# Performance work log

Measured on AMD Instinct MI355X. Metric: run time of the kernel, lower is better.

The kernel has to match this reference:

```python
import jax, jax.numpy as jnp
import numpy as np

NUM_CLASSES = 3
IMG = 448
STRIDES = (8, 16, 32)
POS_IOU, NEG_IOU = 0.5, 0.3
NEG_RATIO = 3
B, T = 64, 20


def _make_anchors(stride):
    f = IMG // stride
    cs = (np.arange(f, dtype=np.float32) + 0.5) * stride
    cx, cy = np.meshgrid(cs, cs, indexing='xy')            # [f, f]
    sizes = np.array([2.0, 2.5, 3.0], np.float32) * stride  # 3 square anchors / loc
    cx = np.broadcast_to(cx[..., None], (f, f, 3))
    cy = np.broadcast_to(cy[..., None], (f, f, 3))
    w = np.broadcast_to(sizes, (f, f, 3))
    boxes = np.stack([cx - w / 2, cy - w / 2, cx + w / 2, cy + w / 2], -1)
    return jnp.asarray(boxes.reshape(-1, 4), jnp.float32)   # [f*f*3, 4]


def setup_inputs() -> dict:
    key = jax.random.key(0)
    k1, k2, k3, kc, ks, kl = jax.random.split(key, 6)
    pred1 = jax.random.normal(k1, (B, 24, 56, 56), jnp.float32)
    pred2 = jax.random.normal(k2, (B, 24, 28, 28), jnp.float32)
    pred3 = jax.random.normal(k3, (B, 24, 14, 14), jnp.float32)
    ctr = jax.random.uniform(kc, (B, T, 2), jnp.float32, 20.0, IMG - 20.0)
    wh = jax.random.uniform(ks, (B, T, 2), jnp.float32, 20.0, 120.0)
    target_boxes = jnp.concatenate([ctr - wh / 2, ctr + wh / 2], axis=-1)  # [B,T,4] xyxy
    target_labels = jax.random.randint(kl, (B, T), 1, NUM_CLASSES + 1, jnp.int32)
    return {
        'pred1': pred1, 'pred2': pred2, 'pred3': pred3,
        'anchor1': _make_anchors(8), 'anchor2': _make_anchors(16), 'anchor3': _make_anchors(32),
        'target_boxes': target_boxes, 'target_labels': target_labels,
    }


def _iou(a, b):  # a [A,4], b [T,4] -> [A,T]
    lt = jnp.maximum(a[:, None, :2], b[None, :, :2])
    rb = jnp.minimum(a[:, None, 2:], b[None, :, 2:])
    wh = jnp.clip(rb - lt, 0.0)
    inter = wh[..., 0] * wh[..., 1]
    area_a = (a[:, 2] - a[:, 0]) * (a[:, 3] - a[:, 1])
    area_b = (b[:, 2] - b[:, 0]) * (b[:, 3] - b[:, 1])
    return inter / (area_a[:, None] + area_b[None, :] - inter + 1e-9)


def _encode(gt, an):  # both [A,4] xyxy -> [A,4] deltas
    aw, ah = an[:, 2] - an[:, 0], an[:, 3] - an[:, 1]
    acx, acy = (an[:, 0] + an[:, 2]) * 0.5, (an[:, 1] + an[:, 3]) * 0.5
    gw, gh = gt[:, 2] - gt[:, 0], gt[:, 3] - gt[:, 1]
    gcx, gcy = (gt[:, 0] + gt[:, 2]) * 0.5, (gt[:, 1] + gt[:, 3]) * 0.5
    return jnp.stack([(gcx - acx) / aw, (gcy - acy) / ah,
                      jnp.log(gw / aw), jnp.log(gh / ah)], axis=-1)


def _bce_logits(x, y):
    return jnp.maximum(x, 0.0) - x * y + jnp.log1p(jnp.exp(-jnp.abs(x)))


def _image_loss(deltas, obj, cls, boxes, labels, anchors):
    # deltas [A,4], obj [A], cls [A,K], boxes [T,4], labels [T], anchors [A,4]
    iou = _iou(anchors, boxes)                    # [A,T]
    matched_t = jnp.argmax(iou, axis=1)           # [A]
    max_iou = jnp.max(iou, axis=1)
    pos = max_iou >= POS_IOU
    neg = max_iou < NEG_IOU
    # force each GT's best anchor to be positive
    best_a = jnp.argmax(iou, axis=0)              # [T]
    matched_t = matched_t.at[best_a].set(jnp.arange(boxes.shape[0]))
    pos = pos.at[best_a].set(True)
    neg = neg.at[best_a].set(False)
    matched_labels = jnp.where(pos, labels[matched_t], 0)
    # objectness + hard negative mining (rank-based topk, jit-safe)
    obj_t = (matched_labels > 0).astype(obj.dtype)
    bce = _bce_logits(obj, obj_t)
    num_pos = pos.sum()
    need = jnp.minimum(NEG_RATIO * num_pos, neg.sum())
    rank = jnp.argsort(jnp.argsort(-jnp.where(neg, bce, -jnp.inf)))
    sel = pos | ((rank < need) & neg)
    obj_loss = jnp.sum(jnp.where(sel, bce, 0.0)) / jnp.maximum(sel.sum(), 1)
    # classification (mean over positives)
    logp = jax.nn.log_softmax(cls, axis=-1)
    tgt = jnp.maximum(matched_labels - 1, 0)
    ce = -jnp.take_along_axis(logp, tgt[:, None], axis=1)[:, 0]
    cls_loss = jnp.sum(jnp.where(pos, ce, 0.0)) / jnp.maximum(num_pos, 1)
    # localization: smooth L1, mean over positive anchor elements
    tdel = _encode(boxes[matched_t], anchors)
    d = jnp.abs(deltas - tdel)
    sl1 = jnp.where(d < 1.0, 0.5 * d * d, d - 0.5)
    loc_loss = jnp.sum(jnp.where(pos[:, None], sl1, 0.0)) / jnp.maximum(4 * num_pos, 1)
    return obj_loss, cls_loss, loc_loss


def _scale_loss(pred, anchors, boxes, labels):
    Bp, C, H, W = pred.shape
    p = pred.transpose(0, 2, 3, 1).reshape(Bp, H * W * 3, 5 + NUM_CLASSES)
    deltas, obj, cls = p[..., :4], p[..., 4], p[..., 5:]
    fn = jax.vmap(lambda d, o, c, b, l: _image_loss(d, o, c, b, l, anchors))
    ol, cl, ll = fn(deltas, obj, cls, boxes, labels)
    return ol.sum(), cl.sum(), ll.sum()


def reference(pred1, pred2, pred3, anchor1, anchor2, anchor3, target_boxes, target_labels):
    tot = jnp.zeros(3, jnp.float32)
    for pred, anc in ((pred1, anchor1), (pred2, anchor2), (pred3, anchor3)):
        ol, cl, ll = _scale_loss(pred, anc, target_boxes, target_labels)
        tot = tot + jnp.stack([ol, cl, ll])
    bsz = target_boxes.shape[0]
    obj, cls, loc = tot[0] / bsz, tot[1] / bsz, tot[2] / bsz
    total = obj + cls + 2.0 * loc
    return jnp.stack([obj, cls, loc, total])
```

## Files before the change

kernel.cpp:

```cpp
#include <hip/hip_runtime.h>
#include <math.h>

#define T 20
#define APB 12348
#define LOSS_OFF 16
#define NPNN_OFF 640
#define KEY_OFF  2048
#define MF_BYTE_OFF (4 * (KEY_OFF + 64 * APB))

__device__ __forceinline__ unsigned mapf(float x) {
    unsigned u = __float_as_uint(x);
    return (u & 0x80000000u) ? ~u : (u | 0x80000000u);
}
__device__ __forceinline__ float unmapf(unsigned m) {
    return __uint_as_float((m & 0x80000000u) ? (m ^ 0x80000000u) : ~m);
}
__device__ __forceinline__ float bce_pos(float x) {
    return fmaxf(x, 0.f) - x + log1pf(expf(-fabsf(x)));
}
__device__ __forceinline__ float bce_neg(float x) {
    return fmaxf(x, 0.f) + log1pf(expf(-fabsf(x)));
}

__global__ __launch_bounds__(256) void match_kernel(
    const float* __restrict__ pred1, const float* __restrict__ pred2,
    const float* __restrict__ pred3, const float* __restrict__ tboxes,
    unsigned* __restrict__ wsu, unsigned short* __restrict__ mf)
{
#pragma clang fp contract(off)
    const int blk = blockIdx.x;
    const int b = blk / 11, c = blk - 11 * b;
    int s, j0;
    if (c < 8)       { s = 0; j0 = c * 1176; }
    else if (c < 10) { s = 1; j0 = (c - 8) * 1176; }
    else             { s = 2; j0 = 0; }
    const float* __restrict__ pred = (s == 0) ? pred1 : (s == 1) ? pred2 : pred3;
    const int W = 56 >> s, HW = W * W, A = 3 * HW;
    const float stf = (float)(8 << s);
    const int sh = 3 - s;
    const int lim = min(1176, A - j0);

    __shared__ float4   s_box[T];
    __shared__ float    s_ab[T];
    __shared__ unsigned s_np[4];
    const int tid = threadIdx.x, lane = tid & 63, wid = tid >> 6;

    if (tid < T) {
        float4 g = ((const float4*)tboxes)[b * T + tid];
        s_box[tid] = g;
        s_ab[tid]  = (g.z - g.x) * (g.w - g.y);
    }
    __syncthreads();

    float ax[5], ay[5], az[5], aw[5], ar[5], bn[5], bu[5];
    int at_[5], kk[5], pp[5];
    bool vv[5];
    float xlo = 1e30f, xhi = -1e30f, ylo = 1e30f, yhi = -1e30f;
    const int obase = 5 * tid;
#pragma unroll
    for (int r = 0; r < 5; r++) {
        int o = obase + r;
        vv[r] = (o < lim);
        int j = j0 + (vv[r] ? o : 0);
        int k   = (j >= HW) + (j >= 2 * HW);
        int pix = j - k * HW;
        int qq  = pix >> sh;
        int py  = (qq * 9363) >> 16;
        int px  = pix - py * W;
        float w  = (2.0f + 0.5f * (float)k) * stf;
        float cx = ((float)px + 0.5f) * stf;
        float cy = ((float)py + 0.5f) * stf;
        ax[r] = cx - 0.5f * w; ay[r] = cy - 0.5f * w;
        az[r] = cx + 0.5f * w; aw[r] = cy + 0.5f * w;
        ar[r] = w * w;
        bn[r] = 0.f; bu[r] = 1.f; at_[r] = 0;
        kk[r] = k; pp[r] = pix;
        xlo = fminf(xlo, ax[r]); xhi = fmaxf(xhi, az[r]);
        ylo = fminf(ylo, ay[r]); yhi = fmaxf(yhi, aw[r]);
    }

    for (int t = 0; t < T; t++) {
        float4 g = s_box[t];
        if (g.x < xhi && g.z > xlo && g.y < yhi && g.w > ylo) {
            float ab = s_ab[t];
#pragma unroll
            for (int r = 0; r < 5; r++) {
                float lx = fmaxf(ax[r], g.x), ly = fmaxf(ay[r], g.y);
                float rx = fminf(az[r], g.z), ry = fminf(aw[r], g.w);
                float ww = fmaxf(rx - lx, 0.f), hh = fmaxf(ry - ly, 0.f);
                float inter = ww * hh;
                float u = ((ar[r] + ab) - inter) + 1e-9f;
                if (inter * bu[r] > bn[r] * u) { bn[r] = inter; bu[r] = u; at_[r] = t; }
            }
        }
    }

    const float* objbase = pred + (size_t)(b * 24 + 4) * HW;
    const unsigned base = (unsigned)(b * APB + ((s == 0) ? 0 : (s == 1) ? 9408 : 11760));
    unsigned npnn = 0;
#pragma unroll
    for (int r = 0; r < 5; r++) {
        if (vv[r]) {
            int j = j0 + obase + r;
            bool pos = (bn[r] + bn[r] >= bu[r]);
            bool neg = (bn[r] < 0.3f * bu[r]);
            unsigned key = 0u;
            if (neg) key = mapf(objbase[(size_t)kk[r] * 8 * HW + pp[r]]);
            wsu[KEY_OFF + base + j] = key;
            mf[base + j] = (unsigned short)(at_[r] | (pos ? 0x100 : 0) | (neg ? 0x200 : 0));
            npnn += (pos ? 1u : 0u) + (neg ? 0x10000u : 0u);
        }
    }
    for (int off = 32; off; off >>= 1) npnn += (unsigned)__shfl_down((int)npnn, off, 64);
    if (lane == 0) s_np[wid] = npnn;
    __syncthreads();
    if (tid == 0) wsu[NPNN_OFF + blk] = s_np[0] + s_np[1] + s_np[2] + s_np[3];
}

__global__ __launch_bounds__(1024) void select_loss_kernel(
    const float* __restrict__ pred1, const float* __restrict__ pred2,
    const float* __restrict__ pred3, const float* __restrict__ tboxes,
    const int* __restrict__ tlabels,
    unsigned* __restrict__ wsu, unsigned short* __restrict__ mf)
{
#pragma clang fp contract(off)
    const int bid = blockIdx.x;
    const int b = bid / 3, s = bid - 3 * b;
    const float* __restrict__ pred = (s == 0) ? pred1 : (s == 1) ? pred2 : pred3;
    const int W = 56 >> s, HW = W * W, A = 3 * HW;
    const float stf = (float)(8 << s);
    const int sh = 3 - s;
    const unsigned base = (unsigned)(b * APB + ((s == 0) ? 0 : (s == 1) ? 9408 : 11760));

    __shared__ float4   s_box[T];
    __shared__ int      s_lab[T];
    __shared__ int      s_besta[T];
    __shared__ unsigned s_misc[4];
    __shared__ float    s_redf[16 * 4];
    __shared__ unsigned hist[2048];

    const int tid = threadIdx.x, lane = tid & 63, wid = tid >> 6;

    if (tid < T) {
        s_box[tid] = ((const float4*)tboxes)[b * T + tid];
        s_lab[tid] = tlabels[b * T + tid];
    }
    if (tid >= 32 && tid < 36) s_misc[tid - 32] = 0;
    __syncthreads();

    for (int t = wid; t < T; t += 16) {
        float4 g = s_box[t];
        float  ab = (g.z - g.x) * (g.w - g.y);
        int px0 = max(0, (int)floorf(g.x / stf) - 2);
        int px1 = min(W - 1, (int)floorf(g.z / stf) + 2);
        int py0 = max(0, (int)floorf(g.y / stf) - 2);
        int py1 = min(W - 1, (int)floorf(g.w / stf) + 2);
        int rowlen = (px1 - px0 + 1) * 3;
        float bi = -1.f, bu2 = 1.f;
        int ba = 0;
        for (int py = py0; py <= py1; py++) {
            float cy = ((float)py + 0.5f) * stf;
            for (int cc = lane; cc < rowlen; cc += 64) {
                int ix = (cc * 21846) >> 16;
                int k  = cc - 3 * ix;
                int px = px0 + ix;
                float w  = (2.0f + 0.5f * (float)k) * stf;
                float cx = ((float)px + 0.5f) * stf;
                float lx = fmaxf(cx - 0.5f * w, g.x), ly = fmaxf(cy - 0.5f * w, g.y);
                float rx = fminf(cx + 0.5f * w, g.z), ry = fminf(cy + 0.5f * w, g.w);
                float ww = fmaxf(rx - lx, 0.f), hh = fmaxf(ry - ly, 0.f);
                float inter = ww * hh;
                float u = ((w * w + ab) - inter) + 1e-9f;
                if (inter * bu2 > bi * u) {
                    bi = inter; bu2 = u; ba = (py * W + px) * 3 + k;
                }
            }
        }
        for (int off = 32; off; off >>= 1) {
            float oi = __shfl_down(bi, off, 64);
            float ou = __shfl_down(bu2, off, 64);
            int   oa = __shfl_down(ba, off, 64);
            float l = oi * bu2, r = bi * ou;
            if (l > r || (l == r && oa < ba)) { bi = oi; bu2 = ou; ba = oa; }
        }
        if (lane == 0) s_besta[t] = ba;
    }
    __syncthreads();

    int  j20 = 0; bool winner = false;
    if (tid < T) {
        int a = s_besta[tid];
        winner = true; bool first = true;
        for (int t2 = tid + 1; t2 < T; t2++) if (s_besta[t2] == a) winner = false;
        for (int t2 = 0; t2 < tid; t2++)     if (s_besta[t2] == a) first  = false;
        int pix = (a * 21846) >> 16;
        int k = a - 3 * pix;
        j20 = k * HW + pix;
        if (first) {
            unsigned old = mf[base + j20];
            unsigned d = ((old & 0x100u) ? 0u : 1u) +
                         ((old & 0x200u) ? 0xFFFF0000u : 0u);
            atomicAdd(&s_misc[0], d);
        }
    }
    __syncthreads();
    if (tid < T && winner) {
        mf[base + j20] = (unsigned short)(tid | 0x100);
        wsu[KEY_OFF + base + j20] = 0u;
    }
    __threadfence_block();
    __syncthreads();

    if (tid == 0) {
        int nslots = (s == 0) ? 8 : (s == 1) ? 2 : 1;
        int sb = b * 11 + ((s == 0) ? 0 : (s == 1) ? 8 : 10);
        unsigned p = 0;
        for (int i = 0; i < nslots; i++) p += wsu[NPNN_OFF + sb + i];
        s_misc[1] = p;
    }
    __syncthreads();
    unsigned packed = s_misc[1] + s_misc[0];
    unsigned np = packed & 0xFFFFu, nn = packed >> 16;
    unsigned need = min(3u * np, nn);

    unsigned keyreg[10];
    unsigned short mfr[10];
#pragma unroll
    for (int m = 0; m < 10; m++) {
        int j = tid + m * 1024;
        keyreg[m] = (j < A) ? wsu[KEY_OFF + base + j] : 0u;
        mfr[m]    = (j < A) ? mf[base + j] : (unsigned short)0;
    }

    unsigned kth = 0xFFFFFFFFu;
    if (need > 0) {
        unsigned prefix = 0, remaining = need;
        const int shifts[3] = {21, 10, 0};
        const int nbits[3]  = {11, 11, 10};
        for (int p = 0; p < 3; p++) {
            const int NB = 1 << nbits[p];
            const int sh_ = shifts[p];
            for (int i = tid; i < NB; i += 1024) hist[i] = 0;
            __syncthreads();
#pragma unroll
            for (int m = 0; m < 10; m++) {
                unsigned k = keyreg[m];
                bool ok = (p == 0) || ((k >> (sh_ + nbits[p])) == prefix);
                if (ok) atomicAdd(&hist[(k >> sh_) & (NB - 1)], 1u);
            }
            __syncthreads();
            if (wid == 0) {
                const int C = NB >> 6;
                int b0 = lane * C;
                unsigned csum = 0;
                for (int i = 0; i < C; i++) csum += hist[b0 + i];
                unsigned Tv = csum;
                for (int off = 1; off < 64; off <<= 1) {
                    unsigned o = __shfl_down(Tv, off, 64);
                    if (lane + off < 64) Tv += o;
                }
                unsigned long long ball = __ballot(Tv >= remaining);
                int L = 63 - __clzll(ball);
                if (lane == L) {
                    unsigned sv = Tv - csum;
                    int bb = b0 + C - 1;
                    while (true) { sv += hist[bb]; if (sv >= remaining) break; bb--; }
                    s_misc[1] = (unsigned)bb;
                    s_misc[2] = sv - hist[bb];
                }
            }
            __syncthreads();
            unsigned B = s_misc[1];
            remaining -= s_misc[2];
            prefix = (prefix << nbits[p]) | B;
        }
        kth = prefix;
    }

    float obj_s = 0.f, cls_s = 0.f, loc_s = 0.f;
    unsigned cgt = 0;
#pragma unroll 1
    for (int m = 0; m < 10; m++) {
        int j = tid + m * 1024;
        if (j >= A) break;
        unsigned mfv = mfr[m];
        if (mfv & 0x100u) {
            int k   = (j >= HW) + (j >= 2 * HW);
            int pix = j - k * HW;
            const float* bp = pred + (size_t)(b * 24 + k * 8) * HW + pix;
            float x = bp[(size_t)4 * HW];
            obj_s += bce_pos(x);
            int t = mfv & 0xFFu;
            float4 g = s_box[t];
            int tgt = s_lab[t] - 1;
            float c0 = bp[(size_t)5 * HW], c1 = bp[(size_t)6 * HW], c2 = bp[(size_t)7 * HW];
            float mm  = fmaxf(c0, fmaxf(c1, c2));
            float lse = logf(expf(c0 - mm) + expf(c1 - mm) + expf(c2 - mm));
            float ct = (tgt == 0) ? c0 : (tgt == 1) ? c1 : c2;
            cls_s += (mm + lse) - ct;
            int qq = pix >> sh;
            int py = (qq * 9363) >> 16;
            int px = pix - py * W;
            float w  = (2.0f + 0.5f * (float)k) * stf;
            float cx = ((float)px + 0.5f) * stf;
            float cy = ((float)py + 0.5f) * stf;
            float gcx = (g.x + g.z) * 0.5f, gcy = (g.y + g.w) * 0.5f;
            float gw = g.z - g.x, gh = g.w - g.y;
            float t0 = (gcx - cx) / w, t1 = (gcy - cy) / w;
            float t2 = logf(gw / w),   t3 = logf(gh / w);
            float d0 = bp[0], d1 = bp[(size_t)HW], d2 = bp[(size_t)2 * HW], d3 = bp[(size_t)3 * HW];
            float dd;
            dd = fabsf(d0 - t0); loc_s += (dd < 1.f) ? 0.5f * dd * dd : dd - 0.5f;
            dd = fabsf(d1 - t1); loc_s += (dd < 1.f) ? 0.5f * dd * dd : dd - 0.5f;
            dd = fabsf(d2 - t2); loc_s += (dd < 1.f) ? 0.5f * dd * dd : dd - 0.5f;
            dd = fabsf(d3 - t3); loc_s += (dd < 1.f) ? 0.5f * dd * dd : dd - 0.5f;
        } else {
            unsigned key = keyreg[m];
            if (key > kth) { obj_s += bce_neg(unmapf(key)); cgt++; }
        }
    }
    for (int off = 32; off; off >>= 1) {
        obj_s += __shfl_down(obj_s, off, 64);
        cls_s += __shfl_down(cls_s, off, 64);
        loc_s += __shfl_down(loc_s, off, 64);
        cgt   += (unsigned)__shfl_down((int)cgt, off, 64);
    }
    if (lane == 0) {
        s_redf[wid * 4 + 0] = obj_s;
        s_redf[wid * 4 + 1] = cls_s;
        s_redf[wid * 4 + 2] = loc_s;
        s_redf[wid * 4 + 3] = __uint_as_float(cgt);
    }
    __syncthreads();
    if (tid == 0) {
        float ob = 0.f, cl = 0.f, lc = 0.f;
        unsigned cg = 0;
        for (int w2 = 0; w2 < 16; w2++) {
            ob += s_redf[w2 * 4 + 0];
            cl += s_redf[w2 * 4 + 1];
            lc += s_redf[w2 * 4 + 2];
            cg += __float_as_uint(s_redf[w2 * 4 + 3]);
        }
        if (need > 0) ob += (float)(need - cg) * bce_neg(unmapf(kth));
        float* wsf = (float*)wsu;
        wsf[LOSS_OFF + bid * 3 + 0] = ob / (float)max(np + need, 1u);
        wsf[LOSS_OFF + bid * 3 + 1] = cl / (float)max(np, 1u);
        wsf[LOSS_OFF + bid * 3 + 2] = lc / (float)max(4u * np, 1u);
    }
}

__global__ void finalize_kernel(const float* __restrict__ wsf,
                                float* __restrict__ out) {
    const int t = threadIdx.x, lane = t & 63, wid = t >> 6;
    __shared__ float red[12];
    float v0 = 0.f, v1 = 0.f, v2 = 0.f;
    if (t < 192) {
        v0 = wsf[LOSS_OFF + 3 * t];
        v1 = wsf[LOSS_OFF + 3 * t + 1];
        v2 = wsf[LOSS_OFF + 3 * t + 2];
    }
    for (int off = 32; off; off >>= 1) {
        v0 += __shfl_down(v0, off, 64);
        v1 += __shfl_down(v1, off, 64);
        v2 += __shfl_down(v2, off, 64);
    }
    if (lane == 0) { red[wid * 3] = v0; red[wid * 3 + 1] = v1; red[wid * 3 + 2] = v2; }
    __syncthreads();
    if (t == 0) {
        float obj = 0.f, cls = 0.f, loc = 0.f;
        for (int w2 = 0; w2 < 4; w2++) {
            obj += red[w2 * 3]; cls += red[w2 * 3 + 1]; loc += red[w2 * 3 + 2];
        }
        obj /= 64.f; cls /= 64.f; loc /= 64.f;
        out[0] = obj; out[1] = cls; out[2] = loc;
        out[3] = obj + cls + 2.f * loc;
    }
}

extern "C" void kernel_launch(void* const* d_in, const int* in_sizes, int n_in,
                              void* d_out, int out_size, void* d_ws, size_t ws_size,
                              hipStream_t stream) {
    const float* pred1   = (const float*)d_in[0];
    const float* pred2   = (const float*)d_in[1];
    const float* pred3   = (const float*)d_in[2];
    const float* tboxes  = (const float*)d_in[6];
    const int*   tlabels = (const int*)d_in[7];
    unsigned* wsu = (unsigned*)d_ws;
    unsigned short* mf = (unsigned short*)((char*)d_ws + MF_BYTE_OFF);
    float* out = (float*)d_out;

    match_kernel<<<64 * 11, 256, 0, stream>>>(pred1, pred2, pred3, tboxes, wsu, mf);
    select_loss_kernel<<<64 * 3, 1024, 0, stream>>>(
        pred1, pred2, pred3, tboxes, tlabels, wsu, mf);
    finalize_kernel<<<1, 256, 0, stream>>>((const float*)d_ws, out);
}
```

Baseline: 124.3 us.

## Fuse anchor matching into select-loss kernel, keeping match results in registers

The separate match kernel is folded into the per-(image,scale) select/loss kernel. Each of the 1024 threads now computes IoU matching for up to 10 anchors and keeps keys and match flags in registers. This removes the global workspace round-trip for keys and flags and one kernel launch. Forced best-anchor matches are applied by comparing against a register copy of the per-target best anchors instead of doing global read-modify-writes. In exchange, matching parallelism drops from 704 blocks of 256 threads to 192 blocks of 1024, so the scale-0 blocks carry much more matching work and the per-block load is more imbalanced.

```diff
diff --git a/kernel.cpp b/kernel.cpp
--- a/kernel.cpp
+++ b/kernel.cpp
@@ -2,126 +2,26 @@
 #include <math.h>
 
 #define T 20
-#define APB 12348
 #define LOSS_OFF 16
-#define NPNN_OFF 640
-#define KEY_OFF  2048
-#define MF_BYTE_OFF (4 * (KEY_OFF + 64 * APB))
-
-__device__ __forceinline__ unsigned mapf(float x) {
+
+static __device__ __forceinline__ unsigned mapf(float x) {
     unsigned u = __float_as_uint(x);
     return (u & 0x80000000u) ? ~u : (u | 0x80000000u);
 }
-__device__ __forceinline__ float unmapf(unsigned m) {
+static __device__ __forceinline__ float unmapf(unsigned m) {
     return __uint_as_float((m & 0x80000000u) ? (m ^ 0x80000000u) : ~m);
 }
-__device__ __forceinline__ float bce_pos(float x) {
+static __device__ __forceinline__ float bce_pos(float x) {
     return fmaxf(x, 0.f) - x + log1pf(expf(-fabsf(x)));
 }
-__device__ __forceinline__ float bce_neg(float x) {
+static __device__ __forceinline__ float bce_neg(float x) {
     return fmaxf(x, 0.f) + log1pf(expf(-fabsf(x)));
 }
 
-__global__ __launch_bounds__(256) void match_kernel(
+__global__ __launch_bounds__(1024, 1) void fused_kernel(
     const float* __restrict__ pred1, const float* __restrict__ pred2,
     const float* __restrict__ pred3, const float* __restrict__ tboxes,
-    unsigned* __restrict__ wsu, unsigned short* __restrict__ mf)
-{
-#pragma clang fp contract(off)
-    const int blk = blockIdx.x;
-    const int b = blk / 11, c = blk - 11 * b;
-    int s, j0;
-    if (c < 8)       { s = 0; j0 = c * 1176; }
-    else if (c < 10) { s = 1; j0 = (c - 8) * 1176; }
-    else             { s = 2; j0 = 0; }
-    const float* __restrict__ pred = (s == 0) ? pred1 : (s == 1) ? pred2 : pred3;
-    const int W = 56 >> s, HW = W * W, A = 3 * HW;
-    const float stf = (float)(8 << s);
-    const int sh = 3 - s;
-    const int lim = min(1176, A - j0);
-
-    __shared__ float4   s_box[T];
-    __shared__ float    s_ab[T];
-    __shared__ unsigned s_np[4];
-    const int tid = threadIdx.x, lane = tid & 63, wid = tid >> 6;
-
-    if (tid < T) {
-        float4 g = ((const float4*)tboxes)[b * T + tid];
-        s_box[tid] = g;
-        s_ab[tid]  = (g.z - g.x) * (g.w - g.y);
-    }
-    __syncthreads();
-
-    float ax[5], ay[5], az[5], aw[5], ar[5], bn[5], bu[5];
-    int at_[5], kk[5], pp[5];
-    bool vv[5];
-    float xlo = 1e30f, xhi = -1e30f, ylo = 1e30f, yhi = -1e30f;
-    const int obase = 5 * tid;
-#pragma unroll
-    for (int r = 0; r < 5; r++) {
-        int o = obase + r;
-        vv[r] = (o < lim);
-        int j = j0 + (vv[r] ? o : 0);
-        int k   = (j >= HW) + (j >= 2 * HW);
-        int pix = j - k * HW;
-        int qq  = pix >> sh;
-        int py  = (qq * 9363) >> 16;
-        int px  = pix - py * W;
-        float w  = (2.0f + 0.5f * (float)k) * stf;
-        float cx = ((float)px + 0.5f) * stf;
-        float cy = ((float)py + 0.5f) * stf;
-        ax[r] = cx - 0.5f * w; ay[r] = cy - 0.5f * w;
-        az[r] = cx + 0.5f * w; aw[r] = cy + 0.5f * w;
-        ar[r] = w * w;
-        bn[r] = 0.f; bu[r] = 1.f; at_[r] = 0;
-        kk[r] = k; pp[r] = pix;
-        xlo = fminf(xlo, ax[r]); xhi = fmaxf(xhi, az[r]);
-        ylo = fminf(ylo, ay[r]); yhi = fmaxf(yhi, aw[r]);
-    }
-
-    for (int t = 0; t < T; t++) {
-        float4 g = s_box[t];
-        if (g.x < xhi && g.z > xlo && g.y < yhi && g.w > ylo) {
-            float ab = s_ab[t];
-#pragma unroll
-            for (int r = 0; r < 5; r++) {
-                float lx = fmaxf(ax[r], g.x), ly = fmaxf(ay[r], g.y);
-                float rx = fminf(az[r], g.z), ry = fminf(aw[r], g.w);
-                float ww = fmaxf(rx - lx, 0.f), hh = fmaxf(ry - ly, 0.f);
-                float inter = ww * hh;
-                float u = ((ar[r] + ab) - inter) + 1e-9f;
-                if (inter * bu[r] > bn[r] * u) { bn[r] = inter; bu[r] = u; at_[r] = t; }
-            }
-        }
-    }
-
-    const float* objbase = pred + (size_t)(b * 24 + 4) * HW;
-    const unsigned base = (unsigned)(b * APB + ((s == 0) ? 0 : (s == 1) ? 9408 : 11760));
-    unsigned npnn = 0;
-#pragma unroll
-    for (int r = 0; r < 5; r++) {
-        if (vv[r]) {
-            int j = j0 + obase + r;
-            bool pos = (bn[r] + bn[r] >= bu[r]);
-            bool neg = (bn[r] < 0.3f * bu[r]);
-            unsigned key = 0u;
-            if (neg) key = mapf(objbase[(size_t)kk[r] * 8 * HW + pp[r]]);
-            wsu[KEY_OFF + base + j] = key;
-            mf[base + j] = (unsigned short)(at_[r] | (pos ? 0x100 : 0) | (neg ? 0x200 : 0));
-            npnn += (pos ? 1u : 0u) + (neg ? 0x10000u : 0u);
-        }
-    }
-    for (int off = 32; off; off >>= 1) npnn += (unsigned)__shfl_down((int)npnn, off, 64);
-    if (lane == 0) s_np[wid] = npnn;
-    __syncthreads();
-    if (tid == 0) wsu[NPNN_OFF + blk] = s_np[0] + s_np[1] + s_np[2] + s_np[3];
-}
-
-__global__ __launch_bounds__(1024) void select_loss_kernel(
-    const float* __restrict__ pred1, const float* __restrict__ pred2,
-    const float* __restrict__ pred3, const float* __restrict__ tboxes,
-    const int* __restrict__ tlabels,
-    unsigned* __restrict__ wsu, unsigned short* __restrict__ mf)
+    const int* __restrict__ tlabels, float* __restrict__ wsf)
 {
 #pragma clang fp contract(off)
     const int bid = blockIdx.x;
@@ -130,27 +30,97 @@
     const int W = 56 >> s, HW = W * W, A = 3 * HW;
     const float stf = (float)(8 << s);
     const int sh = 3 - s;
-    const unsigned base = (unsigned)(b * APB + ((s == 0) ? 0 : (s == 1) ? 9408 : 11760));
 
     __shared__ float4   s_box[T];
+    __shared__ float    s_ab[T];
     __shared__ int      s_lab[T];
     __shared__ int      s_besta[T];
-    __shared__ unsigned s_misc[4];
+    __shared__ unsigned s_npnn;
+    __shared__ unsigned s_bc[2];
     __shared__ float    s_redf[16 * 4];
     __shared__ unsigned hist[2048];
 
     const int tid = threadIdx.x, lane = tid & 63, wid = tid >> 6;
 
     if (tid < T) {
-        s_box[tid] = ((const float4*)tboxes)[b * T + tid];
+        float4 g = ((const float4*)tboxes)[b * T + tid];
+        s_box[tid] = g;
+        s_ab[tid]  = (g.z - g.x) * (g.w - g.y);
         s_lab[tid] = tlabels[b * T + tid];
     }
-    if (tid >= 32 && tid < 36) s_misc[tid - 32] = 0;
-    __syncthreads();
+    if (tid == 0) s_npnn = 0u;
+    __syncthreads();
+
+    const float* objbase = pred + (size_t)(b * 24 + 4) * HW;
+
+    unsigned keyreg[10];
+    unsigned mfr[10];
+#pragma unroll
+    for (int m = 0; m < 10; m++) { keyreg[m] = 0u; mfr[m] = 0u; }
+
+#pragma unroll
+    for (int bat = 0; bat < 2; bat++) {
+        int jb = bat * 5120 + 5 * tid;
+        if (jb < A) {
+            float ax[5], ay[5], az[5], aw[5], ar[5], bn[5], bu[5];
+            int at_[5];
+            float xlo = 1e30f, xhi = -1e30f, ylo = 1e30f, yhi = -1e30f;
+#pragma unroll
+            for (int r = 0; r < 5; r++) {
+                int j = jb + r; if (j >= A) j = A - 1;
+                int k   = (j >= HW) + (j >= 2 * HW);
+                int pix = j - k * HW;
+                int qq  = pix >> sh;
+                int py  = (qq * 9363) >> 16;
+                int px  = pix - py * W;
+                float w  = (2.0f + 0.5f * (float)k) * stf;
+                float cx = ((float)px + 0.5f) * stf;
+                float cy = ((float)py + 0.5f) * stf;
+                ax[r] = cx - 0.5f * w; ay[r] = cy - 0.5f * w;
+                az[r] = cx + 0.5f * w; aw[r] = cy + 0.5f * w;
+                ar[r] = w * w;
+                bn[r] = 0.f; bu[r] = 1.f; at_[r] = 0;
+                xlo = fminf(xlo, ax[r]); xhi = fmaxf(xhi, az[r]);
+                ylo = fminf(ylo, ay[r]); yhi = fmaxf(yhi, aw[r]);
+            }
+            for (int t = 0; t < T; t++) {
+                float4 g = s_box[t];
+                if (g.x < xhi && g.z > xlo && g.y < yhi && g.w > ylo) {
+                    float ab = s_ab[t];
+#pragma unroll
+                    for (int r = 0; r < 5; r++) {
+                        float lx = fmaxf(ax[r], g.x), ly = fmaxf(ay[r], g.y);
+                        float rx = fminf(az[r], g.z), ry = fminf(aw[r], g.w);
+                        float ww = fmaxf(rx - lx, 0.f), hh = fmaxf(ry - ly, 0.f);
+                        float inter = ww * hh;
+                        float u = ((ar[r] + ab) - inter) + 1e-9f;
+                        if (inter * bu[r] > bn[r] * u) {
+                            bn[r] = inter; bu[r] = u; at_[r] = t;
+                        }
+                    }
+                }
+            }
+#pragma unroll
+            for (int r = 0; r < 5; r++) {
+                int j = jb + r;
+                if (j < A) {
+                    int k   = (j >= HW) + (j >= 2 * HW);
+                    int pix = j - k * HW;
+                    bool pos = (bn[r] + bn[r] >= bu[r]);
+                    bool neg = (bn[r] < 0.3f * bu[r]);
+                    unsigned key = 0u;
+                    if (neg) key = mapf(objbase[(size_t)k * 8 * HW + pix]);
+                    keyreg[bat * 5 + r] = key;
+                    mfr[bat * 5 + r] = (unsigned)at_[r] | (pos ? 0x100u : 0u)
+                                                        | (neg ? 0x200u : 0u);
+                }
+            }
+        }
+    }
 
     for (int t = wid; t < T; t += 16) {
         float4 g = s_box[t];
-        float  ab = (g.z - g.x) * (g.w - g.y);
+        float  ab = s_ab[t];
         int px0 = max(0, (int)floorf(g.x / stf) - 2);
         int px1 = min(W - 1, (int)floorf(g.z / stf) + 2);
         int py0 = max(0, (int)floorf(g.y / stf) - 2);
@@ -183,54 +153,38 @@
             float l = oi * bu2, r = bi * ou;
             if (l > r || (l == r && oa < ba)) { bi = oi; bu2 = ou; ba = oa; }
         }
-        if (lane == 0) s_besta[t] = ba;
-    }
-    __syncthreads();
-
-    int  j20 = 0; bool winner = false;
-    if (tid < T) {
-        int a = s_besta[tid];
-        winner = true; bool first = true;
-        for (int t2 = tid + 1; t2 < T; t2++) if (s_besta[t2] == a) winner = false;
-        for (int t2 = 0; t2 < tid; t2++)     if (s_besta[t2] == a) first  = false;
-        int pix = (a * 21846) >> 16;
-        int k = a - 3 * pix;
-        j20 = k * HW + pix;
-        if (first) {
-            unsigned old = mf[base + j20];
-            unsigned d = ((old & 0x100u) ? 0u : 1u) +
-                         ((old & 0x200u) ? 0xFFFF0000u : 0u);
-            atomicAdd(&s_misc[0], d);
-        }
-    }
-    __syncthreads();
-    if (tid < T && winner) {
-        mf[base + j20] = (unsigned short)(tid | 0x100);
-        wsu[KEY_OFF + base + j20] = 0u;
-    }
-    __threadfence_block();
-    __syncthreads();
-
-    if (tid == 0) {
-        int nslots = (s == 0) ? 8 : (s == 1) ? 2 : 1;
-        int sb = b * 11 + ((s == 0) ? 0 : (s == 1) ? 8 : 10);
-        unsigned p = 0;
-        for (int i = 0; i < nslots; i++) p += wsu[NPNN_OFF + sb + i];
-        s_misc[1] = p;
-    }
-    __syncthreads();
-    unsigned packed = s_misc[1] + s_misc[0];
+        if (lane == 0) {
+            int pix = (ba * 21846) >> 16;
+            int k = ba - 3 * pix;
+            s_besta[t] = k * HW + pix;
+        }
+    }
+    __syncthreads();
+
+    {
+        int best[T];
+#pragma unroll
+        for (int t = 0; t < T; t++) best[t] = s_besta[t];
+#pragma unroll
+        for (int m = 0; m < 10; m++) {
+            int j = (m / 5) * 5120 + 5 * tid + (m - (m / 5) * 5);
+            int twin = -1;
+#pragma unroll
+            for (int t = 0; t < T; t++) if (best[t] == j) twin = t;
+            if (twin >= 0) { mfr[m] = (unsigned)twin | 0x100u; keyreg[m] = 0u; }
+        }
+    }
+
+    unsigned npnn = 0;
+#pragma unroll
+    for (int m = 0; m < 10; m++)
+        npnn += ((mfr[m] >> 8) & 1u) + (((mfr[m] >> 9) & 1u) << 16);
+    for (int off = 32; off; off >>= 1) npnn += (unsigned)__shfl_down((int)npnn, off, 64);
+    if (lane == 0) atomicAdd(&s_npnn, npnn);
+    __syncthreads();
+    unsigned packed = s_npnn;
     unsigned np = packed & 0xFFFFu, nn = packed >> 16;
     unsigned need = min(3u * np, nn);
-
-    unsigned keyreg[10];
-    unsigned short mfr[10];
-#pragma unroll
-    for (int m = 0; m < 10; m++) {
-        int j = tid + m * 1024;
-        keyreg[m] = (j < A) ? wsu[KEY_OFF + base + j] : 0u;
-        mfr[m]    = (j < A) ? mf[base + j] : (unsigned short)0;
-    }
 
     unsigned kth = 0xFFFFFFFFu;
     if (need > 0) {
@@ -265,13 +219,13 @@
                     unsigned sv = Tv - csum;
                     int bb = b0 + C - 1;
                     while (true) { sv += hist[bb]; if (sv >= remaining) break; bb--; }
-                    s_misc[1] = (unsigned)bb;
-                    s_misc[2] = sv - hist[bb];
+                    s_bc[0] = (unsigned)bb;
+                    s_bc[1] = sv - hist[bb];
                 }
             }
             __syncthreads();
-            unsigned B = s_misc[1];
-            remaining -= s_misc[2];
+            unsigned B = s_bc[0];
+            remaining -= s_bc[1];
             prefix = (prefix << nbits[p]) | B;
         }
         kth = prefix;
@@ -279,44 +233,45 @@
 
     float obj_s = 0.f, cls_s = 0.f, loc_s = 0.f;
     unsigned cgt = 0;
-#pragma unroll 1
+#pragma unroll
     for (int m = 0; m < 10; m++) {
-        int j = tid + m * 1024;
-        if (j >= A) break;
-        unsigned mfv = mfr[m];
-        if (mfv & 0x100u) {
-            int k   = (j >= HW) + (j >= 2 * HW);
-            int pix = j - k * HW;
-            const float* bp = pred + (size_t)(b * 24 + k * 8) * HW + pix;
-            float x = bp[(size_t)4 * HW];
-            obj_s += bce_pos(x);
-            int t = mfv & 0xFFu;
-            float4 g = s_box[t];
-            int tgt = s_lab[t] - 1;
-            float c0 = bp[(size_t)5 * HW], c1 = bp[(size_t)6 * HW], c2 = bp[(size_t)7 * HW];
-            float mm  = fmaxf(c0, fmaxf(c1, c2));
-            float lse = logf(expf(c0 - mm) + expf(c1 - mm) + expf(c2 - mm));
-            float ct = (tgt == 0) ? c0 : (tgt == 1) ? c1 : c2;
-            cls_s += (mm + lse) - ct;
-            int qq = pix >> sh;
-            int py = (qq * 9363) >> 16;
-            int px = pix - py * W;
-            float w  = (2.0f + 0.5f * (float)k) * stf;
-            float cx = ((float)px + 0.5f) * stf;
-            float cy = ((float)py + 0.5f) * stf;
-            float gcx = (g.x + g.z) * 0.5f, gcy = (g.y + g.w) * 0.5f;
-            float gw = g.z - g.x, gh = g.w - g.y;
-            float t0 = (gcx - cx) / w, t1 = (gcy - cy) / w;
-            float t2 = logf(gw / w),   t3 = logf(gh / w);
-            float d0 = bp[0], d1 = bp[(size_t)HW], d2 = bp[(size_t)2 * HW], d3 = bp[(size_t)3 * HW];
-            float dd;
-            dd = fabsf(d0 - t0); loc_s += (dd < 1.f) ? 0.5f * dd * dd : dd - 0.5f;
-            dd = fabsf(d1 - t1); loc_s += (dd < 1.f) ? 0.5f * dd * dd : dd - 0.5f;
-            dd = fabsf(d2 - t2); loc_s += (dd < 1.f) ? 0.5f * dd * dd : dd - 0.5f;
-            dd = fabsf(d3 - t3); loc_s += (dd < 1.f) ? 0.5f * dd * dd : dd - 0.5f;
-        } else {
-            unsigned key = keyreg[m];
-            if (key > kth) { obj_s += bce_neg(unmapf(key)); cgt++; }
+        int j = (m / 5) * 5120 + 5 * tid + (m - (m / 5) * 5);
+        if (j < A) {
+            unsigned mfv = mfr[m];
+            if (mfv & 0x100u) {
+                int k   = (j >= HW) + (j >= 2 * HW);
+                int pix = j - k * HW;
+                const float* bp = pred + (size_t)(b * 24 + k * 8) * HW + pix;
+                float x = bp[(size_t)4 * HW];
+                obj_s += bce_pos(x);
+                int t = mfv & 0xFFu;
+                float4 g = s_box[t];
+                int tgt = s_lab[t] - 1;
+                float c0 = bp[(size_t)5 * HW], c1 = bp[(size_t)6 * HW], c2 = bp[(size_t)7 * HW];
+                float mm  = fmaxf(c0, fmaxf(c1, c2));
+                float lse = logf(expf(c0 - mm) + expf(c1 - mm) + expf(c2 - mm));
+                float ct = (tgt == 0) ? c0 : (tgt == 1) ? c1 : c2;
+                cls_s += (mm + lse) - ct;
+                int qq = pix >> sh;
+                int py = (qq * 9363) >> 16;
+                int px = pix - py * W;
+                float w  = (2.0f + 0.5f * (float)k) * stf;
+                float cx = ((float)px + 0.5f) * stf;
+                float cy = ((float)py + 0.5f) * stf;
+                float gcx = (g.x + g.z) * 0.5f, gcy = (g.y + g.w) * 0.5f;
+                float gw = g.z - g.x, gh = g.w - g.y;
+                float t0 = (gcx - cx) / w, t1 = (gcy - cy) / w;
+                float t2 = logf(gw / w),   t3 = logf(gh / w);
+                float d0 = bp[0], d1 = bp[(size_t)HW], d2 = bp[(size_t)2 * HW], d3 = bp[(size_t)3 * HW];
+                float dd;
+                dd = fabsf(d0 - t0); loc_s += (dd < 1.f) ? 0.5f * dd * dd : dd - 0.5f;
+                dd = fabsf(d1 - t1); loc_s += (dd < 1.f) ? 0.5f * dd * dd : dd - 0.5f;
+                dd = fabsf(d2 - t2); loc_s += (dd < 1.f) ? 0.5f * dd * dd : dd - 0.5f;
+                dd = fabsf(d3 - t3); loc_s += (dd < 1.f) ? 0.5f * dd * dd : dd - 0.5f;
+            } else {
+                unsigned key = keyreg[m];
+                if (key > kth) { obj_s += bce_neg(unmapf(key)); cgt++; }
+            }
         }
     }
     for (int off = 32; off; off >>= 1) {
@@ -342,7 +297,6 @@
             cg += __float_as_uint(s_redf[w2 * 4 + 3]);
         }
         if (need > 0) ob += (float)(need - cg) * bce_neg(unmapf(kth));
-        float* wsf = (float*)wsu;
         wsf[LOSS_OFF + bid * 3 + 0] = ob / (float)max(np + need, 1u);
         wsf[LOSS_OFF + bid * 3 + 1] = cl / (float)max(np, 1u);
         wsf[LOSS_OFF + bid * 3 + 2] = lc / (float)max(4u * np, 1u);
@@ -385,12 +339,10 @@
     const float* pred3   = (const float*)d_in[2];
     const float* tboxes  = (const float*)d_in[6];
     const int*   tlabels = (const int*)d_in[7];
-    unsigned* wsu = (unsigned*)d_ws;
-    unsigned short* mf = (unsigned short*)((char*)d_ws + MF_BYTE_OFF);
+    float* wsf = (float*)d_ws;
     float* out = (float*)d_out;
 
-    match_kernel<<<64 * 11, 256, 0, stream>>>(pred1, pred2, pred3, tboxes, wsu, mf);
-    select_loss_kernel<<<64 * 3, 1024, 0, stream>>>(
-        pred1, pred2, pred3, tboxes, tlabels, wsu, mf);
-    finalize_kernel<<<1, 256, 0, stream>>>((const float*)d_ws, out);
-}
+    fused_kernel<<<64 * 3, 1024, 0, stream>>>(
+        pred1, pred2, pred3, tboxes, tlabels, wsf);
+    finalize_kernel<<<1, 256, 0, stream>>>(wsf, out);
+}
```

Result: faster. 120.7 us (-2.9%).

## Stage keys and flags in LDS, recount positives locally, use 8-bit radix select

Applied to the files above, without the earlier changes.

The select/loss kernel now copies each image-scale's keys and match flags into shared memory and applies the forced best-anchor overrides there, instead of writing them back to global memory. Positive and negative counts are recomputed from the shared flags, so the match kernel no longer does its block reduction and no longer writes per-block counts. The radix select for the k-th negative becomes four 8-bit passes with per-wave-pair histograms, which cuts atomic contention. The block size drops to 512 threads. This adds about 56KB of LDS per block, which may limit occupancy, and each pass now scans shared memory rather than registers.

```diff
diff --git a/kernel.cpp b/kernel.cpp
--- a/kernel.cpp
+++ b/kernel.cpp
@@ -2,23 +2,23 @@
 #include <math.h>
 
 #define T 20
+#define MAXA 9408
 #define APB 12348
 #define LOSS_OFF 16
-#define NPNN_OFF 640
 #define KEY_OFF  2048
 #define MF_BYTE_OFF (4 * (KEY_OFF + 64 * APB))
 
-__device__ __forceinline__ unsigned mapf(float x) {
+static __device__ __forceinline__ unsigned mapf(float x) {
     unsigned u = __float_as_uint(x);
     return (u & 0x80000000u) ? ~u : (u | 0x80000000u);
 }
-__device__ __forceinline__ float unmapf(unsigned m) {
+static __device__ __forceinline__ float unmapf(unsigned m) {
     return __uint_as_float((m & 0x80000000u) ? (m ^ 0x80000000u) : ~m);
 }
-__device__ __forceinline__ float bce_pos(float x) {
+static __device__ __forceinline__ float bce_pos(float x) {
     return fmaxf(x, 0.f) - x + log1pf(expf(-fabsf(x)));
 }
-__device__ __forceinline__ float bce_neg(float x) {
+static __device__ __forceinline__ float bce_neg(float x) {
     return fmaxf(x, 0.f) + log1pf(expf(-fabsf(x)));
 }
 
@@ -40,10 +40,9 @@
     const int sh = 3 - s;
     const int lim = min(1176, A - j0);
 
-    __shared__ float4   s_box[T];
-    __shared__ float    s_ab[T];
-    __shared__ unsigned s_np[4];
-    const int tid = threadIdx.x, lane = tid & 63, wid = tid >> 6;
+    __shared__ float4 s_box[T];
+    __shared__ float  s_ab[T];
+    const int tid = threadIdx.x;
 
     if (tid < T) {
         float4 g = ((const float4*)tboxes)[b * T + tid];
@@ -97,7 +96,6 @@
 
     const float* objbase = pred + (size_t)(b * 24 + 4) * HW;
     const unsigned base = (unsigned)(b * APB + ((s == 0) ? 0 : (s == 1) ? 9408 : 11760));
-    unsigned npnn = 0;
 #pragma unroll
     for (int r = 0; r < 5; r++) {
         if (vv[r]) {
@@ -108,20 +106,16 @@
             if (neg) key = mapf(objbase[(size_t)kk[r] * 8 * HW + pp[r]]);
             wsu[KEY_OFF + base + j] = key;
             mf[base + j] = (unsigned short)(at_[r] | (pos ? 0x100 : 0) | (neg ? 0x200 : 0));
-            npnn += (pos ? 1u : 0u) + (neg ? 0x10000u : 0u);
-        }
-    }
-    for (int off = 32; off; off >>= 1) npnn += (unsigned)__shfl_down((int)npnn, off, 64);
-    if (lane == 0) s_np[wid] = npnn;
-    __syncthreads();
-    if (tid == 0) wsu[NPNN_OFF + blk] = s_np[0] + s_np[1] + s_np[2] + s_np[3];
-}
-
-__global__ __launch_bounds__(1024) void select_loss_kernel(
+        }
+    }
+}
+
+__global__ __launch_bounds__(512) void select_loss_kernel(
     const float* __restrict__ pred1, const float* __restrict__ pred2,
     const float* __restrict__ pred3, const float* __restrict__ tboxes,
     const int* __restrict__ tlabels,
-    unsigned* __restrict__ wsu, unsigned short* __restrict__ mf)
+    const unsigned* __restrict__ wsu, const unsigned short* __restrict__ mf,
+    float* __restrict__ wsf)
 {
 #pragma clang fp contract(off)
     const int bid = blockIdx.x;
@@ -132,25 +126,36 @@
     const int sh = 3 - s;
     const unsigned base = (unsigned)(b * APB + ((s == 0) ? 0 : (s == 1) ? 9408 : 11760));
 
+    __shared__ unsigned       s_key[MAXA];
+    __shared__ unsigned short s_mf[MAXA];
     __shared__ float4   s_box[T];
+    __shared__ float    s_ab[T];
     __shared__ int      s_lab[T];
     __shared__ int      s_besta[T];
-    __shared__ unsigned s_misc[4];
-    __shared__ float    s_redf[16 * 4];
-    __shared__ unsigned hist[2048];
+    __shared__ unsigned whist[4][256];
+    __shared__ unsigned s_npnn;
+    __shared__ unsigned s_bc[2];
+    __shared__ float    s_redf[8 * 4];
 
     const int tid = threadIdx.x, lane = tid & 63, wid = tid >> 6;
 
     if (tid < T) {
-        s_box[tid] = ((const float4*)tboxes)[b * T + tid];
+        float4 g = ((const float4*)tboxes)[b * T + tid];
+        s_box[tid] = g;
+        s_ab[tid]  = (g.z - g.x) * (g.w - g.y);
         s_lab[tid] = tlabels[b * T + tid];
     }
-    if (tid >= 32 && tid < 36) s_misc[tid - 32] = 0;
-    __syncthreads();
-
-    for (int t = wid; t < T; t += 16) {
+    if (tid == 0) s_npnn = 0u;
+    __syncthreads();
+
+    for (int j = tid; j < A; j += 512) {
+        s_key[j] = wsu[KEY_OFF + base + j];
+        s_mf[j]  = mf[base + j];
+    }
+
+    for (int t = wid; t < T; t += 8) {
         float4 g = s_box[t];
-        float  ab = (g.z - g.x) * (g.w - g.y);
+        float  ab = s_ab[t];
         int px0 = max(0, (int)floorf(g.x / stf) - 2);
         int px1 = min(W - 1, (int)floorf(g.z / stf) + 2);
         int py0 = max(0, (int)floorf(g.y / stf) - 2);
@@ -183,77 +188,61 @@
             float l = oi * bu2, r = bi * ou;
             if (l > r || (l == r && oa < ba)) { bi = oi; bu2 = ou; ba = oa; }
         }
-        if (lane == 0) s_besta[t] = ba;
-    }
-    __syncthreads();
-
-    int  j20 = 0; bool winner = false;
+        if (lane == 0) {
+            int pix = (ba * 21846) >> 16;
+            int k = ba - 3 * pix;
+            s_besta[t] = k * HW + pix;
+        }
+    }
+    __syncthreads();
+
     if (tid < T) {
-        int a = s_besta[tid];
-        winner = true; bool first = true;
-        for (int t2 = tid + 1; t2 < T; t2++) if (s_besta[t2] == a) winner = false;
-        for (int t2 = 0; t2 < tid; t2++)     if (s_besta[t2] == a) first  = false;
-        int pix = (a * 21846) >> 16;
-        int k = a - 3 * pix;
-        j20 = k * HW + pix;
-        if (first) {
-            unsigned old = mf[base + j20];
-            unsigned d = ((old & 0x100u) ? 0u : 1u) +
-                         ((old & 0x200u) ? 0xFFFF0000u : 0u);
-            atomicAdd(&s_misc[0], d);
-        }
-    }
-    __syncthreads();
-    if (tid < T && winner) {
-        mf[base + j20] = (unsigned short)(tid | 0x100);
-        wsu[KEY_OFF + base + j20] = 0u;
-    }
-    __threadfence_block();
-    __syncthreads();
-
-    if (tid == 0) {
-        int nslots = (s == 0) ? 8 : (s == 1) ? 2 : 1;
-        int sb = b * 11 + ((s == 0) ? 0 : (s == 1) ? 8 : 10);
-        unsigned p = 0;
-        for (int i = 0; i < nslots; i++) p += wsu[NPNN_OFF + sb + i];
-        s_misc[1] = p;
-    }
-    __syncthreads();
-    unsigned packed = s_misc[1] + s_misc[0];
-    unsigned np = packed & 0xFFFFu, nn = packed >> 16;
+        int j20 = s_besta[tid];
+        bool winner = true;
+        for (int t2 = tid + 1; t2 < T; t2++) if (s_besta[t2] == j20) winner = false;
+        if (winner) {
+            s_mf[j20]  = (unsigned short)(tid | 0x100);
+            s_key[j20] = 0u;
+        }
+    }
+    __syncthreads();
+
+    unsigned npnn = 0;
+    for (int j = tid; j < A; j += 512) {
+        unsigned m = s_mf[j];
+        npnn += ((m >> 8) & 1u) + (((m >> 9) & 1u) << 16);
+    }
+    for (int off = 32; off; off >>= 1) npnn += (unsigned)__shfl_down((int)npnn, off, 64);
+    if (lane == 0) atomicAdd(&s_npnn, npnn);
+    __syncthreads();
+    unsigned np = s_npnn & 0xFFFFu, nn = s_npnn >> 16;
     unsigned need = min(3u * np, nn);
-
-    unsigned keyreg[10];
-    unsigned short mfr[10];
-#pragma unroll
-    for (int m = 0; m < 10; m++) {
-        int j = tid + m * 1024;
-        keyreg[m] = (j < A) ? wsu[KEY_OFF + base + j] : 0u;
-        mfr[m]    = (j < A) ? mf[base + j] : (unsigned short)0;
-    }
 
     unsigned kth = 0xFFFFFFFFu;
     if (need > 0) {
         unsigned prefix = 0, remaining = need;
-        const int shifts[3] = {21, 10, 0};
-        const int nbits[3]  = {11, 11, 10};
-        for (int p = 0; p < 3; p++) {
-            const int NB = 1 << nbits[p];
-            const int sh_ = shifts[p];
-            for (int i = tid; i < NB; i += 1024) hist[i] = 0;
+        for (int p = 0; p < 4; p++) {
+            const int sh_ = 24 - 8 * p;
+            if (tid < 256) {
+                whist[0][tid] = 0; whist[1][tid] = 0;
+                whist[2][tid] = 0; whist[3][tid] = 0;
+            }
             __syncthreads();
-#pragma unroll
-            for (int m = 0; m < 10; m++) {
-                unsigned k = keyreg[m];
-                bool ok = (p == 0) || ((k >> (sh_ + nbits[p])) == prefix);
-                if (ok) atomicAdd(&hist[(k >> sh_) & (NB - 1)], 1u);
+            for (int j = tid; j < A; j += 512) {
+                unsigned k = s_key[j];
+                bool ok = (p == 0) || ((k >> (sh_ + 8)) == prefix);
+                if (ok) atomicAdd(&whist[wid >> 1][(k >> sh_) & 255u], 1u);
+            }
+            __syncthreads();
+            if (tid < 256) {
+                whist[0][tid] = whist[0][tid] + whist[1][tid]
+                              + whist[2][tid] + whist[3][tid];
             }
             __syncthreads();
             if (wid == 0) {
-                const int C = NB >> 6;
-                int b0 = lane * C;
-                unsigned csum = 0;
-                for (int i = 0; i < C; i++) csum += hist[b0 + i];
+                int b0 = lane * 4;
+                unsigned csum = whist[0][b0] + whist[0][b0 + 1]
+                              + whist[0][b0 + 2] + whist[0][b0 + 3];
                 unsigned Tv = csum;
                 for (int off = 1; off < 64; off <<= 1) {
                     unsigned o = __shfl_down(Tv, off, 64);
@@ -263,27 +252,23 @@
                 int L = 63 - __clzll(ball);
                 if (lane == L) {
                     unsigned sv = Tv - csum;
-                    int bb = b0 + C - 1;
-                    while (true) { sv += hist[bb]; if (sv >= remaining) break; bb--; }
-                    s_misc[1] = (unsigned)bb;
-                    s_misc[2] = sv - hist[bb];
+                    int bb = b0 + 3;
+                    while (true) { sv += whist[0][bb]; if (sv >= remaining) break; bb--; }
+                    s_bc[0] = (unsigned)bb;
+                    s_bc[1] = sv - whist[0][bb];
                 }
             }
             __syncthreads();
-            unsigned B = s_misc[1];
-            remaining -= s_misc[2];
-            prefix = (prefix << nbits[p]) | B;
+            remaining -= s_bc[1];
+            prefix = (prefix << 8) | s_bc[0];
         }
         kth = prefix;
     }
 
     float obj_s = 0.f, cls_s = 0.f, loc_s = 0.f;
     unsigned cgt = 0;
-#pragma unroll 1
-    for (int m = 0; m < 10; m++) {
-        int j = tid + m * 1024;
-        if (j >= A) break;
-        unsigned mfv = mfr[m];
+    for (int j = tid; j < A; j += 512) {
+        unsigned mfv = s_mf[j];
         if (mfv & 0x100u) {
             int k   = (j >= HW) + (j >= 2 * HW);
             int pix = j - k * HW;
@@ -315,7 +300,7 @@
             dd = fabsf(d2 - t2); loc_s += (dd < 1.f) ? 0.5f * dd * dd : dd - 0.5f;
             dd = fabsf(d3 - t3); loc_s += (dd < 1.f) ? 0.5f * dd * dd : dd - 0.5f;
         } else {
-            unsigned key = keyreg[m];
+            unsigned key = s_key[j];
             if (key > kth) { obj_s += bce_neg(unmapf(key)); cgt++; }
         }
     }
@@ -335,14 +320,13 @@
     if (tid == 0) {
         float ob = 0.f, cl = 0.f, lc = 0.f;
         unsigned cg = 0;
-        for (int w2 = 0; w2 < 16; w2++) {
+        for (int w2 = 0; w2 < 8; w2++) {
             ob += s_redf[w2 * 4 + 0];
             cl += s_redf[w2 * 4 + 1];
             lc += s_redf[w2 * 4 + 2];
             cg += __float_as_uint(s_redf[w2 * 4 + 3]);
         }
         if (need > 0) ob += (float)(need - cg) * bce_neg(unmapf(kth));
-        float* wsf = (float*)wsu;
         wsf[LOSS_OFF + bid * 3 + 0] = ob / (float)max(np + need, 1u);
         wsf[LOSS_OFF + bid * 3 + 1] = cl / (float)max(np, 1u);
         wsf[LOSS_OFF + bid * 3 + 2] = lc / (float)max(4u * np, 1u);
@@ -387,10 +371,11 @@
     const int*   tlabels = (const int*)d_in[7];
     unsigned* wsu = (unsigned*)d_ws;
     unsigned short* mf = (unsigned short*)((char*)d_ws + MF_BYTE_OFF);
+    float* wsf = (float*)d_ws;
     float* out = (float*)d_out;
 
     match_kernel<<<64 * 11, 256, 0, stream>>>(pred1, pred2, pred3, tboxes, wsu, mf);
-    select_loss_kernel<<<64 * 3, 1024, 0, stream>>>(
-        pred1, pred2, pred3, tboxes, tlabels, wsu, mf);
-    finalize_kernel<<<1, 256, 0, stream>>>((const float*)d_ws, out);
-}
+    select_loss_kernel<<<64 * 3, 512, 0, stream>>>(
+        pred1, pred2, pred3, tboxes, tlabels, wsu, mf, wsf);
+    finalize_kernel<<<1, 256, 0, stream>>>(wsf, out);
+}
```

New measurement: 135.1 us. 1.09x slower.
